# Kernel tuning notes

Hardware: AMD Instinct MI355X
Metric: run time of the kernel (lower is better)

## Reference

```python
import jax, jax.numpy as jnp
import numpy as np

B, IN, COND, H, LAT, E, GH = 8192, 256, 1024, 1024, 128, 6, 64
INP = LAT + COND      # decoder layer0 input size = 1152
INTER = LAT + H       # decoder layer1/2 input size = 1152


def setup_inputs() -> dict:
    key = jax.random.key(0)
    ks = jax.random.split(key, 30)
    n = lambda k, shape, s=0.02: jax.random.normal(k, shape, dtype=jnp.float32) * s
    return {
        'x': jax.random.normal(ks[0], (B, IN), dtype=jnp.float32),
        'y': jax.random.normal(ks[1], (B, COND), dtype=jnp.float32),
        'eps': jax.random.normal(ks[2], (B, LAT), dtype=jnp.float32),
        # encoder: layer k input = prev_dim + IN (x is re-concatenated each layer)
        'enc_w0': n(ks[3], (IN + COND + IN, H)), 'enc_b0': jnp.zeros((H,), jnp.float32),
        'enc_w1': n(ks[4], (H + IN, H)),         'enc_b1': jnp.zeros((H,), jnp.float32),
        'mu_w': n(ks[5], (H, LAT)),  'mu_b': jnp.zeros((LAT,), jnp.float32),
        'lv_w': n(ks[6], (H, LAT)),  'lv_b': jnp.zeros((LAT,), jnp.float32),
        # gating network (input = latent + cond)
        'g_w0': n(ks[7], (INP, GH)), 'g_b0': jnp.zeros((GH,), jnp.float32),
        'g_w1': n(ks[8], (GH, GH)),  'g_b1': jnp.zeros((GH,), jnp.float32),
        'g_w2': n(ks[9], (GH, E)),   'g_b2': jnp.zeros((E,), jnp.float32),
        # expert weights [E, in, out] and biases [E, out] (bias init 0.01 as in source)
        'exp_w0': n(ks[10], (E, INP, H)),   'exp_b0': jnp.full((E, H), 0.01, jnp.float32),
        'exp_w1': n(ks[11], (E, INTER, H)), 'exp_b1': jnp.full((E, H), 0.01, jnp.float32),
        'exp_w2': n(ks[12], (E, INTER, IN)), 'exp_b2': jnp.full((E, IN), 0.01, jnp.float32),
    }


def _forward(x, y, eps, enc_w0, enc_b0, enc_w1, enc_b1, mu_w, mu_b, lv_w, lv_b,
             g_w0, g_b0, g_w1, g_b1, g_w2, g_b2,
             exp_w0, exp_b0, exp_w1, exp_b1, exp_w2, exp_b2):
    elu = jax.nn.elu
    # --- Encoder ---
    h = jnp.concatenate([x, y], axis=1)
    h = elu(jnp.concatenate([h, x], axis=1) @ enc_w0 + enc_b0)
    h = elu(jnp.concatenate([h, x], axis=1) @ enc_w1 + enc_b1)
    mu = h @ mu_w + mu_b
    logvar = h @ lv_w + lv_b
    # --- Reparameterize (eps passed explicitly for determinism) ---
    z = mu + eps * jnp.exp(0.5 * logvar)
    # --- MixedDecoder ---
    g = jnp.concatenate([z, y], axis=1)
    g = elu(g @ g_w0 + g_b0)
    g = elu(g @ g_w1 + g_b1)
    coeff = jax.nn.softmax(g @ g_w2 + g_b2, axis=1)  # [B, E]
    layer_out = y
    for W, bb, act in ((exp_w0, exp_b0, True), (exp_w1, exp_b1, True), (exp_w2, exp_b2, False)):
        inp = jnp.concatenate([z, layer_out], axis=1)  # [B, I]
        # fused mixture-of-experts projection: avoids materializing per-sample [B,I,O] weight
        out = coeff @ bb + jnp.einsum('be,bi,eio->bo', coeff, inp, W)
        layer_out = elu(out) if act else out
    return layer_out, mu, logvar


def reference(x, y, eps, enc_w0, enc_b0, enc_w1, enc_b1, mu_w, mu_b, lv_w, lv_b,
              g_w0, g_b0, g_w1, g_b1, g_w2, g_b2,
              exp_w0, exp_b0, exp_w1, exp_b1, exp_w2, exp_b2):
    return _forward(x, y, eps, enc_w0, enc_b0, enc_w1, enc_b1, mu_w, mu_b, lv_w, lv_b,
                    g_w0, g_b0, g_w1, g_b1, g_w2, g_b2,
                    exp_w0, exp_b0, exp_w1, exp_b1, exp_w2, exp_b2)
```

## Files before the change

kernel.cpp:

```cpp
#include <hip/hip_runtime.h>
#include <hip/hip_bf16.h>
#include <cstddef>

using u16 = unsigned short;
using short8 = __attribute__((ext_vector_type(8))) short;
using f32x4 = __attribute__((ext_vector_type(4))) float;

constexpr int B_   = 8192;
constexpr int IN_  = 256;
constexpr int COND_= 1024;
constexpr int H_   = 1024;
constexpr int LAT_ = 128;
constexpr int NE_  = 6;
constexpr int GH_  = 64;
constexpr int INP_ = 1152;
constexpr int K0_  = 1536;
constexpr int K1_  = 1280;

constexpr int BK = 64;

typedef const __attribute__((address_space(1))) void gv_t;
typedef __attribute__((address_space(3))) void lv_t;
#define GLDS(g, l) __builtin_amdgcn_global_load_lds((gv_t*)(g), (lv_t*)(l), 16, 0, 0)

__device__ __forceinline__ u16 f2b(float f) {
  __hip_bfloat16 h = __float2bfloat16(f);
  return *reinterpret_cast<u16*>(&h);
}
__device__ __forceinline__ float elu1(float x) { return x > 0.f ? x : (__expf(x) - 1.f); }

__global__ void k_transpose(const float* __restrict__ in, u16* __restrict__ out,
                            int R, int C, long inStride, long outStride) {
  __shared__ float t[32][33];
  const float* ip = in + (long)blockIdx.z * inStride;
  u16* op = out + (long)blockIdx.z * outStride;
  int c0 = blockIdx.x * 32, r0 = blockIdx.y * 32;
  int tx = threadIdx.x, ty = threadIdx.y;
#pragma unroll
  for (int i = 0; i < 4; i++) {
    int r = r0 + ty + i * 8, c = c0 + tx;
    if (r < R && c < C) t[ty + i * 8][tx] = ip[(long)r * C + c];
  }
  __syncthreads();
#pragma unroll
  for (int i = 0; i < 4; i++) {
    int c = c0 + ty + i * 8, r = r0 + tx;
    if (r < R && c < C) op[(long)c * R + r] = f2b(t[tx][ty + i * 8]);
  }
}

__global__ __launch_bounds__(256) void k_pre(
    const float* __restrict__ enc_w0, const float* __restrict__ enc_w1,
    const float* __restrict__ mu_w, const float* __restrict__ lv_w,
    const float* __restrict__ g_w0, const float* __restrict__ exp_w0,
    const float* __restrict__ x, const float* __restrict__ y,
    u16* __restrict__ encw0T, u16* __restrict__ encw1T, u16* __restrict__ mulvT,
    u16* __restrict__ gw0T, u16* __restrict__ ew0T,
    u16* __restrict__ A0, u16* __restrict__ A1)
{
  __shared__ float t[32][33];
  const int b = blockIdx.x;
  const int tid = threadIdx.x;
  const int tx = tid & 31, ty = tid >> 5;

  auto tr = [&](const float* in, u16* out, int R, int C, int bx, int by) {
    int c0 = bx * 32, r0 = by * 32;
#pragma unroll
    for (int i = 0; i < 4; i++) {
      int r = r0 + ty + i * 8, c = c0 + tx;
      if (r < R && c < C) t[ty + i * 8][tx] = in[(long)r * C + c];
    }
    __syncthreads();
#pragma unroll
    for (int i = 0; i < 4; i++) {
      int c = c0 + ty + i * 8, r = r0 + tx;
      if (r < R && c < C) out[(long)c * R + r] = f2b(t[tx][ty + i * 8]);
    }
  };

  if (b < 1536)       { tr(enc_w0, encw0T, K0_, H_, b & 31, b >> 5); }
  else if (b < 2816)  { int l = b - 1536; tr(enc_w1, encw1T, K1_, H_, l & 31, l >> 5); }
  else if (b < 2944)  { int l = b - 2816; tr(mu_w, mulvT, H_, LAT_, l & 3, l >> 2); }
  else if (b < 3072)  { int l = b - 2944; tr(lv_w, mulvT + (size_t)LAT_ * H_, H_, LAT_, l & 3, l >> 2); }
  else if (b < 3144)  { int l = b - 3072; tr(g_w0, gw0T, INP_, GH_, l & 1, l >> 1); }
  else if (b < 10056) {
    int l = b - 3144, e = l / 1152, r2 = l % 1152;
    tr(exp_w0 + (long)e * INP_ * H_, ew0T + (long)e * INP_ * H_, INP_, H_, r2 & 31, r2 >> 5);
  } else {
    long idx = (long)(b - 10056) * 256 + tid;
    long n0 = (long)B_ * K0_;
    if (idx < n0) {
      int bb = (int)(idx / K0_), c = (int)(idx % K0_);
      float v;
      if (c < IN_)              v = x[(long)bb * IN_ + c];
      else if (c < IN_ + COND_) v = y[(long)bb * COND_ + (c - IN_)];
      else                      v = x[(long)bb * IN_ + (c - IN_ - COND_)];
      A0[idx] = f2b(v);
    } else {
      long j = idx - n0;
      if (j < (long)B_ * IN_) {
        int bb = (int)(j / IN_), c = (int)(j % IN_);
        A1[(long)bb * K1_ + H_ + c] = f2b(x[(long)bb * IN_ + c]);
      }
    }
  }
}

__global__ __launch_bounds__(256) void k_mid(
    const float* __restrict__ exp_w2, u16* __restrict__ ew2T,
    const float* __restrict__ mu, const float* __restrict__ lv,
    const float* __restrict__ eps, const float* __restrict__ y,
    u16* __restrict__ ZY, u16* __restrict__ D1, u16* __restrict__ D2)
{
  __shared__ float t[32][33];
  const int b = blockIdx.x;
  const int tid = threadIdx.x;
  if (b < 1728) {
    const int tx = tid & 31, ty = tid >> 5;
    int e = b / 288, r2 = b % 288;
    const float* in = exp_w2 + (long)e * INP_ * IN_;
    u16* out = ew2T + (long)e * INP_ * IN_;
    int c0 = (r2 & 7) * 32, r0 = (r2 >> 3) * 32;
#pragma unroll
    for (int i = 0; i < 4; i++) {
      int r = r0 + ty + i * 8, c = c0 + tx;
      if (r < INP_ && c < IN_) t[ty + i * 8][tx] = in[(long)r * IN_ + c];
    }
    __syncthreads();
#pragma unroll
    for (int i = 0; i < 4; i++) {
      int c = c0 + ty + i * 8, r = r0 + tx;
      if (r < INP_ && c < IN_) out[(long)c * INP_ + r] = f2b(t[tx][ty + i * 8]);
    }
  } else {
    long idx = (long)(b - 1728) * 256 + tid;
    if (idx >= (long)B_ * INP_) return;
    int bb = (int)(idx / INP_), c = (int)(idx % INP_);
    if (c < LAT_) {
      long o = (long)bb * LAT_ + c;
      float z = mu[o] + eps[o] * __expf(0.5f * lv[o]);
      u16 zb = f2b(z);
      ZY[idx] = zb; D1[idx] = zb; D2[idx] = zb;
    } else {
      ZY[idx] = f2b(y[(long)bb * COND_ + (c - LAT_)]);
    }
  }
}

__global__ __launch_bounds__(256) void k_gate(const float* __restrict__ G1,
    const float* __restrict__ w1, const float* __restrict__ b1,
    const float* __restrict__ w2, const float* __restrict__ b2,
    float* __restrict__ coeff) {
  __shared__ float W1[64][65];
  __shared__ float W2[64][8];
  __shared__ float B1[64], B2[8];
  int tid = threadIdx.x;
  for (int i = tid; i < 64 * 64; i += 256) W1[i >> 6][i & 63] = w1[i];
  for (int i = tid; i < 64 * 6; i += 256) W2[i / 6][i % 6] = w2[i];
  if (tid < 64) B1[tid] = b1[tid];
  if (tid < 8)  B2[tid] = (tid < 6) ? b2[tid] : 0.f;
  __syncthreads();
  int row = blockIdx.x * 256 + tid;
  const float* gr = G1 + (long)row * GH_;
  float g[64];
#pragma unroll
  for (int i = 0; i < 16; i++) {
    float4 v = *(const float4*)(gr + i * 4);
    g[i*4] = v.x; g[i*4+1] = v.y; g[i*4+2] = v.z; g[i*4+3] = v.w;
  }
  float lg[6];
#pragma unroll
  for (int e = 0; e < 6; e++) lg[e] = B2[e];
  for (int n = 0; n < 64; n++) {
    float s = B1[n];
#pragma unroll
    for (int k = 0; k < 64; k++) s += g[k] * W1[k][n];
    s = elu1(s);
#pragma unroll
    for (int e = 0; e < 6; e++) lg[e] += s * W2[n][e];
  }
  float m = lg[0];
#pragma unroll
  for (int e = 1; e < 6; e++) m = fmaxf(m, lg[e]);
  float p[6], sum = 0.f;
#pragma unroll
  for (int e = 0; e < 6; e++) { p[e] = __expf(lg[e] - m); sum += p[e]; }
  float inv = 1.f / sum;
#pragma unroll
  for (int e = 0; e < 6; e++) coeff[(long)row * 6 + e] = p[e] * inv;
}

template<int KSTEPS, int E, bool MOE>
__global__ __launch_bounds__(512, 2) void k_gemm8(
    const u16* __restrict__ A,
    const u16* __restrict__ WT,
    const float* __restrict__ bias,
    const float* __restrict__ coeff,
    int N,
    u16* __restrict__ outH, int ldo)
{
  constexpr int KK = KSTEPS * BK;
  constexpr int T = E * KSTEPS;
  __shared__ __align__(16) u16 As[3][256][BK];
  __shared__ __align__(16) u16 Bs[3][128][BK];
  __shared__ float Cf[MOE ? 256 : 1][8];

  const int tid = threadIdx.x;
  const int lane = tid & 63, w = tid >> 6;
  const int wr = w >> 1, wc = w & 1;
  const int lin = blockIdx.x + blockIdx.y * gridDim.x;
  const int rb  = (lin & 7) * 4 + ((lin >> 3) & 3);
  const int cp  = lin >> 5;
  const int brow = rb * 256, bcol = cp * 128;
  const int lr = lane & 15, hi = lane >> 4;
  const int lk = hi * 8;
  const int xsw = (lr & 7) << 3;

  if (MOE) {
    if (tid < 256) {
#pragma unroll
      for (int e2 = 0; e2 < 8; e2++)
        Cf[tid][e2] = (e2 < 6) ? coeff[(long)(brow + tid) * 6 + e2] : 0.f;
    }
    __syncthreads();
  }

  f32x4 acc[4][4];
#pragma unroll
  for (int m = 0; m < 4; m++)
#pragma unroll
    for (int n = 0; n < 4; n++)
#pragma unroll
      for (int r = 0; r < 4; r++) acc[m][n][r] = 0.f;
  f32x4 pacc[MOE ? 4 : 1][MOE ? 4 : 1];
  if constexpr (MOE) {
#pragma unroll
    for (int m = 0; m < 4; m++)
#pragma unroll
      for (int n = 0; n < 4; n++)
#pragma unroll
        for (int r = 0; r < 4; r++) pacc[m][n][r] = 0.f;
  }

  const int srow = w * 8 + (lane >> 3);
  const int sdst = (lane & 7) * 8;
  const int ssrc = ((lane & 7) ^ ((lane >> 3) & 7)) * 8;
  const u16* Asrc = A + (long)(brow + srow) * KK + ssrc;
  const u16* Bsrc = WT + (long)(bcol + srow) * KK + ssrc;

  auto STAGE_H = [&](int t2, int buf, int h) {
    const int e2 = (E == 1) ? 0 : (t2 / KSTEPS);
    int k2 = (E == 1) ? t2 : (t2 % KSTEPS);
    if (E > 1 && (e2 & 1)) k2 = KSTEPS - 1 - k2;
    const u16* ap = Asrc + (long)k2 * BK;
    const u16* bp = Bsrc + (long)e2 * ((long)N * KK) + (long)k2 * BK;
    GLDS(ap + (long)((h * 2 + 0) * 64) * KK, &As[buf][(h * 2 + 0) * 64 + srow][sdst]);
    GLDS(ap + (long)((h * 2 + 1) * 64) * KK, &As[buf][(h * 2 + 1) * 64 + srow][sdst]);
    GLDS(bp + (long)(h * 64) * KK,           &Bs[buf][h * 64 + srow][sdst]);
  };

  STAGE_H(0, 0, 0); STAGE_H(0, 0, 1);
  STAGE_H(1, 1, 0); STAGE_H(1, 1, 1);
  asm volatile("s_waitcnt vmcnt(6)" ::: "memory");
  asm volatile("s_barrier" ::: "memory");

  for (int t = 0; t < T; ++t) {
    const int cur = t % 3;
    const int nbuf = (t + 2) % 3;
    const bool do_stage = (t + 2 < T);

    {
      short8 af[4], bfr[4];
      const int cc = lk ^ xsw;
#pragma unroll
      for (int m = 0; m < 4; m++)
        af[m] = *(const short8*)&As[cur][wr * 64 + m * 16 + lr][cc];
#pragma unroll
      for (int n = 0; n < 4; n++)
        bfr[n] = *(const short8*)&Bs[cur][wc * 64 + n * 16 + lr][cc];
      if (do_stage) STAGE_H(t + 2, nbuf, 0);
      asm volatile("s_barrier" ::: "memory");
      __builtin_amdgcn_s_setprio(1);
#pragma unroll
      for (int m = 0; m < 4; m++)
#pragma unroll
        for (int n = 0; n < 4; n++) {
          if constexpr (MOE)
            pacc[m][n] = __builtin_amdgcn_mfma_f32_16x16x32_bf16(af[m], bfr[n], pacc[m][n], 0, 0, 0);
          else
            acc[m][n] = __builtin_amdgcn_mfma_f32_16x16x32_bf16(af[m], bfr[n], acc[m][n], 0, 0, 0);
        }
      __builtin_amdgcn_s_setprio(0);
      asm volatile("s_barrier" ::: "memory");
    }

    {
      short8 af[4], bfr[4];
      const int cc = (32 + lk) ^ xsw;
#pragma unroll
      for (int m = 0; m < 4; m++)
        af[m] = *(const short8*)&As[cur][wr * 64 + m * 16 + lr][cc];
#pragma unroll
      for (int n = 0; n < 4; n++)
        bfr[n] = *(const short8*)&Bs[cur][wc * 64 + n * 16 + lr][cc];
      if (do_stage) STAGE_H(t + 2, nbuf, 1);
      asm volatile("s_barrier" ::: "memory");
      __builtin_amdgcn_s_setprio(1);
#pragma unroll
      for (int m = 0; m < 4; m++)
#pragma unroll
        for (int n = 0; n < 4; n++) {
          if constexpr (MOE)
            pacc[m][n] = __builtin_amdgcn_mfma_f32_16x16x32_bf16(af[m], bfr[n], pacc[m][n], 0, 0, 0);
          else
            acc[m][n] = __builtin_amdgcn_mfma_f32_16x16x32_bf16(af[m], bfr[n], acc[m][n], 0, 0, 0);
        }
      __builtin_amdgcn_s_setprio(0);
      if (t + 1 < T) {
        if (do_stage) asm volatile("s_waitcnt vmcnt(6)" ::: "memory");
        else          asm volatile("s_waitcnt vmcnt(0)" ::: "memory");
      }
      asm volatile("s_barrier" ::: "memory");
    }

    if constexpr (MOE) {
      if ((t + 1) % KSTEPS == 0) {
        const int e = t / KSTEPS;
#pragma unroll
        for (int m = 0; m < 4; m++)
#pragma unroll
          for (int r = 0; r < 4; r++) {
            float c = Cf[wr * 64 + m * 16 + hi * 4 + r][e];
#pragma unroll
            for (int n = 0; n < 4; n++) acc[m][n][r] += c * pacc[m][n][r];
          }
        if (t + 1 < T) {
#pragma unroll
          for (int m = 0; m < 4; m++)
#pragma unroll
            for (int n = 0; n < 4; n++)
#pragma unroll
              for (int r = 0; r < 4; r++) pacc[m][n][r] = 0.f;
        }
      }
    }
  }

#pragma unroll
  for (int m = 0; m < 4; m++)
#pragma unroll
    for (int n = 0; n < 4; n++) {
      const int col = bcol + wc * 64 + n * 16 + lr;
#pragma unroll
      for (int r = 0; r < 4; r++) {
        const int rowl = wr * 64 + m * 16 + hi * 4 + r;
        const long row = brow + rowl;
        float v = acc[m][n][r];
        if constexpr (MOE) {
          float bv = 0.f;
#pragma unroll
          for (int e = 0; e < 6; e++) bv += Cf[rowl][e] * bias[(long)e * N + col];
          v += bv;
        } else {
          v += bias[col];
        }
        v = elu1(v);
        outH[row * (long)ldo + col] = f2b(v);
      }
    }
}

template<int KSTEPS, int E, bool MOE>
__global__ __launch_bounds__(256, 2) void k_m2(
    const u16* __restrict__ A,
    const u16* __restrict__ WT,
    const float* __restrict__ bias, const float* __restrict__ bias2,
    const float* __restrict__ coeff,
    int N,
    u16* __restrict__ outH, float* __restrict__ outF, float* __restrict__ outF2,
    int ldo, int splitcol, int act)
{
  constexpr int KK = KSTEPS * BK;
  constexpr int T = E * KSTEPS;
  __shared__ __align__(16) u16 As[3][64][BK];
  __shared__ __align__(16) u16 Bs[3][128][BK];
  __shared__ float Cf[MOE ? 64 : 1][8];

  const int tid = threadIdx.x;
  const int lane = tid & 63, w = tid >> 6;
  const int wr = w >> 1, wc = w & 1;
  const int brow = blockIdx.x * 64, bcol = blockIdx.y * 128;
  const int lr = lane & 15, hi = lane >> 4;
  const int lk = hi * 8;
  const int xsw = (lr & 7) << 3;

  if (MOE) {
    if (tid < 64) {
#pragma unroll
      for (int e2 = 0; e2 < 8; e2++)
        Cf[tid][e2] = (e2 < 6) ? coeff[(long)(brow + tid) * 6 + e2] : 0.f;
    }
    __syncthreads();
  }

  f32x4 acc[2][4];
#pragma unroll
  for (int m = 0; m < 2; m++)
#pragma unroll
    for (int n = 0; n < 4; n++)
#pragma unroll
      for (int r = 0; r < 4; r++) acc[m][n][r] = 0.f;
  f32x4 pacc[MOE ? 2 : 1][MOE ? 4 : 1];
  if constexpr (MOE) {
#pragma unroll
    for (int m = 0; m < 2; m++)
#pragma unroll
      for (int n = 0; n < 4; n++)
#pragma unroll
        for (int r = 0; r < 4; r++) pacc[m][n][r] = 0.f;
  }

  const int srow = w * 8 + (lane >> 3);
  const int sdst = (lane & 7) * 8;
  const int ssrc = ((lane & 7) ^ ((lane >> 3) & 7)) * 8;
  const u16* Asrc = A + (long)(brow + srow) * KK + ssrc;
  const u16* Bsrc = WT + (long)(bcol + srow) * KK + ssrc;

  auto STAGE_H = [&](int t2, int buf, int h) {
    const int e2 = (E == 1) ? 0 : (t2 / KSTEPS);
    int k2 = (E == 1) ? t2 : (t2 % KSTEPS);
    if (E > 1 && (e2 & 1)) k2 = KSTEPS - 1 - k2;
    const u16* ap = Asrc + (long)k2 * BK;
    const u16* bp = Bsrc + (long)e2 * ((long)N * KK) + (long)k2 * BK;
    GLDS(ap + (long)(h * 32) * KK,            &As[buf][h * 32 + srow][sdst]);
    GLDS(bp + (long)(h * 64) * KK,            &Bs[buf][h * 64 + srow][sdst]);
    GLDS(bp + (long)(h * 64 + 32) * KK,       &Bs[buf][h * 64 + 32 + srow][sdst]);
  };

  STAGE_H(0, 0, 0); STAGE_H(0, 0, 1);
  STAGE_H(1, 1, 0); STAGE_H(1, 1, 1);
  asm volatile("s_waitcnt vmcnt(6)" ::: "memory");
  asm volatile("s_barrier" ::: "memory");

  for (int t = 0; t < T; ++t) {
    const int cur = t % 3;
    const int nbuf = (t + 2) % 3;
    const bool do_stage = (t + 2 < T);

    {
      short8 af[2], bfr[4];
      const int cc = lk ^ xsw;
#pragma unroll
      for (int m = 0; m < 2; m++)
        af[m] = *(const short8*)&As[cur][wr * 32 + m * 16 + lr][cc];
#pragma unroll
      for (int n = 0; n < 4; n++)
        bfr[n] = *(const short8*)&Bs[cur][wc * 64 + n * 16 + lr][cc];
      if (do_stage) STAGE_H(t + 2, nbuf, 0);
      asm volatile("s_barrier" ::: "memory");
      __builtin_amdgcn_s_setprio(1);
#pragma unroll
      for (int m = 0; m < 2; m++)
#pragma unroll
        for (int n = 0; n < 4; n++) {
          if constexpr (MOE)
            pacc[m][n] = __builtin_amdgcn_mfma_f32_16x16x32_bf16(af[m], bfr[n], pacc[m][n], 0, 0, 0);
          else
            acc[m][n] = __builtin_amdgcn_mfma_f32_16x16x32_bf16(af[m], bfr[n], acc[m][n], 0, 0, 0);
        }
      __builtin_amdgcn_s_setprio(0);
      asm volatile("s_barrier" ::: "memory");
    }

    {
      short8 af[2], bfr[4];
      const int cc = (32 + lk) ^ xsw;
#pragma unroll
      for (int m = 0; m < 2; m++)
        af[m] = *(const short8*)&As[cur][wr * 32 + m * 16 + lr][cc];
#pragma unroll
      for (int n = 0; n < 4; n++)
        bfr[n] = *(const short8*)&Bs[cur][wc * 64 + n * 16 + lr][cc];
      if (do_stage) STAGE_H(t + 2, nbuf, 1);
      asm volatile("s_barrier" ::: "memory");
      __builtin_amdgcn_s_setprio(1);
#pragma unroll
      for (int m = 0; m < 2; m++)
#pragma unroll
        for (int n = 0; n < 4; n++) {
          if constexpr (MOE)
            pacc[m][n] = __builtin_amdgcn_mfma_f32_16x16x32_bf16(af[m], bfr[n], pacc[m][n], 0, 0, 0);
          else
            acc[m][n] = __builtin_amdgcn_mfma_f32_16x16x32_bf16(af[m], bfr[n], acc[m][n], 0, 0, 0);
        }
      __builtin_amdgcn_s_setprio(0);
      if (t + 1 < T) {
        if (do_stage) asm volatile("s_waitcnt vmcnt(6)" ::: "memory");
        else          asm volatile("s_waitcnt vmcnt(0)" ::: "memory");
      }
      asm volatile("s_barrier" ::: "memory");
    }

    if constexpr (MOE) {
      if ((t + 1) % KSTEPS == 0) {
        const int e = t / KSTEPS;
#pragma unroll
        for (int m = 0; m < 2; m++)
#pragma unroll
          for (int r = 0; r < 4; r++) {
            float c = Cf[wr * 32 + m * 16 + hi * 4 + r][e];
#pragma unroll
            for (int n = 0; n < 4; n++) acc[m][n][r] += c * pacc[m][n][r];
          }
        if (t + 1 < T) {
#pragma unroll
          for (int m = 0; m < 2; m++)
#pragma unroll
            for (int n = 0; n < 4; n++)
#pragma unroll
              for (int r = 0; r < 4; r++) pacc[m][n][r] = 0.f;
        }
      }
    }
  }

#pragma unroll
  for (int m = 0; m < 2; m++)
#pragma unroll
    for (int n = 0; n < 4; n++) {
      const int col = bcol + wc * 64 + n * 16 + lr;
      if (col >= N) continue;
#pragma unroll
      for (int r = 0; r < 4; r++) {
        const int rowl = wr * 32 + m * 16 + hi * 4 + r;
        const long row = brow + rowl;
        float v = acc[m][n][r];
        if constexpr (MOE) {
          float bv = 0.f;
#pragma unroll
          for (int e = 0; e < 6; e++) bv += Cf[rowl][e] * bias[(long)e * N + col];
          v += bv;
        } else {
          v += (col < splitcol) ? bias[col] : bias2[col - splitcol];
        }
        if (act) v = elu1(v);
        if (outH) outH[row * (long)ldo + col] = f2b(v);
        else if (col < splitcol) outF[row * (long)ldo + col] = v;
        else outF2[row * (long)ldo + (col - splitcol)] = v;
      }
    }
}

extern "C" void kernel_launch(void* const* d_in, const int* in_sizes, int n_in,
                              void* d_out, int out_size, void* d_ws, size_t ws_size,
                              hipStream_t stream) {
  (void)in_sizes; (void)out_size;
  if (n_in < 23) return;
  const float* x      = (const float*)d_in[0];
  const float* y      = (const float*)d_in[1];
  const float* eps    = (const float*)d_in[2];
  const float* enc_w0 = (const float*)d_in[3];
  const float* enc_b0 = (const float*)d_in[4];
  const float* enc_w1 = (const float*)d_in[5];
  const float* enc_b1 = (const float*)d_in[6];
  const float* mu_w   = (const float*)d_in[7];
  const float* mu_b   = (const float*)d_in[8];
  const float* lv_w   = (const float*)d_in[9];
  const float* lv_b   = (const float*)d_in[10];
  const float* g_w0   = (const float*)d_in[11];
  const float* g_b0   = (const float*)d_in[12];
  const float* g_w1   = (const float*)d_in[13];
  const float* g_b1   = (const float*)d_in[14];
  const float* g_w2   = (const float*)d_in[15];
  const float* g_b2   = (const float*)d_in[16];
  const float* exp_w0 = (const float*)d_in[17];
  const float* exp_b0 = (const float*)d_in[18];
  const float* exp_w1 = (const float*)d_in[19];
  const float* exp_b1 = (const float*)d_in[20];
  const float* exp_w2 = (const float*)d_in[21];
  const float* exp_b2 = (const float*)d_in[22];

  char* ws = (char*)d_ws;
  size_t off = 0;
  auto alloc = [&](size_t bytes) -> void* {
    void* p = ws + off; off += (bytes + 255) & ~(size_t)255; return p;
  };
  u16* A0     = (u16*)alloc((size_t)B_ * K0_ * 2);
  u16* A1     = (u16*)alloc((size_t)B_ * K1_ * 2);
  u16* H2     = (u16*)alloc((size_t)B_ * H_ * 2);
  u16* ZY     = (u16*)alloc((size_t)B_ * INP_ * 2);
  u16* encw0T = (u16*)alloc((size_t)K0_ * H_ * 2);
  u16* encw1T = (u16*)alloc((size_t)K1_ * H_ * 2);
  u16* mulvT  = (u16*)alloc((size_t)256 * H_ * 2);
  u16* gw0T   = (u16*)alloc((size_t)GH_ * INP_ * 2);
  u16* ew0T   = (u16*)alloc((size_t)NE_ * H_ * INP_ * 2);
  if (ws_size < off) return;

  u16* D1 = A0;
  u16* D2 = A1;
  float* G1    = (float*)H2;
  float* COEFF = (float*)((char*)H2 + (size_t)B_ * GH_ * 4);
  u16* ew2T = (u16*)((char*)H2 + (size_t)4 * 1024 * 1024);
  u16* ew1T = ZY;

  float* outO = (float*)d_out;
  float* muO  = outO + (size_t)B_ * IN_;
  float* lvO  = muO + (size_t)B_ * LAT_;

  k_pre<<<67400, 256, 0, stream>>>(enc_w0, enc_w1, mu_w, lv_w, g_w0, exp_w0,
      x, y, encw0T, encw1T, mulvT, gw0T, ew0T, A0, A1);

  k_gemm8<K0_ / BK, 1, false><<<dim3(32, 8), 512, 0, stream>>>(A0, encw0T, enc_b0,
      nullptr, H_, A1, K1_);
  k_gemm8<K1_ / BK, 1, false><<<dim3(32, 8), 512, 0, stream>>>(A1, encw1T, enc_b1,
      nullptr, H_, H2, H_);

  k_m2<H_ / BK, 1, false><<<dim3(B_ / 64, 2), 256, 0, stream>>>(H2, mulvT,
      mu_b, lv_b, nullptr, 256, nullptr, muO, lvO, LAT_, LAT_, 0);

  k_mid<<<38592, 256, 0, stream>>>(exp_w2, ew2T, muO, lvO, eps, y, ZY, D1, D2);

  k_m2<INP_ / BK, 1, false><<<dim3(B_ / 64, 1), 256, 0, stream>>>(ZY, gw0T,
      g_b0, g_b0, nullptr, GH_, nullptr, G1, nullptr, GH_, GH_, 1);
  k_gate<<<B_ / 256, 256, 0, stream>>>(G1, g_w1, g_b1, g_w2, g_b2, COEFF);

  k_gemm8<INP_ / BK, NE_, true><<<dim3(32, 8), 512, 0, stream>>>(ZY, ew0T, exp_b0,
      COEFF, H_, D1 + LAT_, INP_);
  k_transpose<<<dim3(32, 36, NE_), dim3(32, 8), 0, stream>>>(exp_w1, ew1T, INP_, H_,
                                                    (long)INP_ * H_, (long)INP_ * H_);
  k_gemm8<INP_ / BK, NE_, true><<<dim3(32, 8), 512, 0, stream>>>(D1, ew1T, exp_b1,
      COEFF, H_, D2 + LAT_, INP_);
  k_m2<INP_ / BK, NE_, true><<<dim3(B_ / 64, 2), 256, 0, stream>>>(D2, ew2T,
      exp_b2, nullptr, COEFF, IN_, nullptr, outO, nullptr, IN_, IN_, 0);
}
```

Before: 533.5 us.

## Reorder MoE GEMM loop to share A tile across experts per k-step

The mixture-of-experts GEMM moves the expert loop inside the k loop. Each A tile is loaded into LDS once and reused by all six experts, instead of being reloaded once per expert. The per-expert partial product is scaled by the gating coefficient and added to the accumulator after every k-step, which adds VALU FMAs and a coefficient LDS read per step. A is now double-buffered and B triple-buffered, which changes the LDS footprint and the vmcnt waits.

```diff
diff --git a/kernel.cpp b/kernel.cpp
--- a/kernel.cpp
+++ b/kernel.cpp
@@ -190,8 +190,8 @@
   for (int e = 0; e < 6; e++) coeff[(long)row * 6 + e] = p[e] * inv;
 }
 
-template<int KSTEPS, int E, bool MOE>
-__global__ __launch_bounds__(512, 2) void k_gemm8(
+template<int KSTEPS>
+__global__ __launch_bounds__(512, 2) void k_moe8(
     const u16* __restrict__ A,
     const u16* __restrict__ WT,
     const float* __restrict__ bias,
@@ -200,10 +200,9 @@
     u16* __restrict__ outH, int ldo)
 {
   constexpr int KK = KSTEPS * BK;
-  constexpr int T = E * KSTEPS;
-  __shared__ __align__(16) u16 As[3][256][BK];
+  __shared__ __align__(16) u16 As[2][256][BK];
   __shared__ __align__(16) u16 Bs[3][128][BK];
-  __shared__ float Cf[MOE ? 256 : 1][8];
+  __shared__ float CfT[6][256];
 
   const int tid = threadIdx.x;
   const int lane = tid & 63, w = tid >> 6;
@@ -216,14 +215,11 @@
   const int lk = hi * 8;
   const int xsw = (lr & 7) << 3;
 
-  if (MOE) {
-    if (tid < 256) {
-#pragma unroll
-      for (int e2 = 0; e2 < 8; e2++)
-        Cf[tid][e2] = (e2 < 6) ? coeff[(long)(brow + tid) * 6 + e2] : 0.f;
-    }
-    __syncthreads();
-  }
+  if (tid < 256) {
+#pragma unroll
+    for (int e = 0; e < 6; e++) CfT[e][tid] = coeff[(long)(brow + tid) * 6 + e];
+  }
+  __syncthreads();
 
   f32x4 acc[4][4];
 #pragma unroll
@@ -232,15 +228,8 @@
     for (int n = 0; n < 4; n++)
 #pragma unroll
       for (int r = 0; r < 4; r++) acc[m][n][r] = 0.f;
-  f32x4 pacc[MOE ? 4 : 1][MOE ? 4 : 1];
-  if constexpr (MOE) {
-#pragma unroll
-    for (int m = 0; m < 4; m++)
-#pragma unroll
-      for (int n = 0; n < 4; n++)
-#pragma unroll
-        for (int r = 0; r < 4; r++) pacc[m][n][r] = 0.f;
-  }
+  const f32x4 zf = {0.f, 0.f, 0.f, 0.f};
+  f32x4 pacc[4][4];
 
   const int srow = w * 8 + (lane >> 3);
   const int sdst = (lane & 7) * 8;
@@ -248,12 +237,162 @@
   const u16* Asrc = A + (long)(brow + srow) * KK + ssrc;
   const u16* Bsrc = WT + (long)(bcol + srow) * KK + ssrc;
 
+  auto STAGE_A = [&](int kt2, int abuf2) {
+    const u16* ap = Asrc + (long)kt2 * BK;
+#pragma unroll
+    for (int i = 0; i < 4; i++)
+      GLDS(ap + (long)(i * 64) * KK, &As[abuf2][i * 64 + srow][sdst]);
+  };
+  auto STAGE_B = [&](int e2, int k2, int buf) {
+    const u16* bp = Bsrc + (long)e2 * ((long)N * KK) + (long)k2 * BK;
+    GLDS(bp,                 &Bs[buf][srow][sdst]);
+    GLDS(bp + (long)64 * KK, &Bs[buf][64 + srow][sdst]);
+  };
+
+  STAGE_A(0, 0);
+  STAGE_B(0, 0, 0);
+  STAGE_B(1, 0, 1);
+  asm volatile("s_waitcnt vmcnt(2)" ::: "memory");
+  asm volatile("s_barrier" ::: "memory");
+
+  short8 af[2][4];
+
+  for (int kt = 0; kt < KSTEPS; ++kt) {
+    const int abuf = kt & 1;
+    const bool haveA = (kt + 1 < KSTEPS);
+#pragma unroll
+    for (int g = 0; g < 6; ++g) {
+      const int cur = g % 3;
+      const int nbuf = (g + 2) % 3;
+      const int e2 = (g + 2) % 6;
+      const int k2 = kt + (g >= 4 ? 1 : 0);
+      const bool stageB = (k2 < KSTEPS);
+
+      float4 cg[4];
+      {
+        if (g == 0) {
+#pragma unroll
+          for (int p = 0; p < 2; p++)
+#pragma unroll
+            for (int m = 0; m < 4; m++)
+              af[p][m] = *(const short8*)&As[abuf][wr * 64 + m * 16 + lr][(p * 32 + lk) ^ xsw];
+        }
+#pragma unroll
+        for (int m = 0; m < 4; m++)
+          cg[m] = *(const float4*)&CfT[g][wr * 64 + m * 16 + hi * 4];
+        short8 bfr[4];
+        const int cc0 = lk ^ xsw;
+#pragma unroll
+        for (int n = 0; n < 4; n++)
+          bfr[n] = *(const short8*)&Bs[cur][wc * 64 + n * 16 + lr][cc0];
+        if (stageB) STAGE_B(e2, k2, nbuf);
+        if (g == 2 && haveA) STAGE_A(kt + 1, abuf ^ 1);
+        asm volatile("s_barrier" ::: "memory");
+        __builtin_amdgcn_s_setprio(1);
+#pragma unroll
+        for (int m = 0; m < 4; m++)
+#pragma unroll
+          for (int n = 0; n < 4; n++)
+            pacc[m][n] = __builtin_amdgcn_mfma_f32_16x16x32_bf16(af[0][m], bfr[n], zf, 0, 0, 0);
+        __builtin_amdgcn_s_setprio(0);
+        asm volatile("s_barrier" ::: "memory");
+      }
+      {
+        short8 bfr[4];
+        const int cc1 = (32 + lk) ^ xsw;
+#pragma unroll
+        for (int n = 0; n < 4; n++)
+          bfr[n] = *(const short8*)&Bs[cur][wc * 64 + n * 16 + lr][cc1];
+        asm volatile("s_barrier" ::: "memory");
+        __builtin_amdgcn_s_setprio(1);
+#pragma unroll
+        for (int m = 0; m < 4; m++)
+#pragma unroll
+          for (int n = 0; n < 4; n++)
+            pacc[m][n] = __builtin_amdgcn_mfma_f32_16x16x32_bf16(af[1][m], bfr[n], pacc[m][n], 0, 0, 0);
+        __builtin_amdgcn_s_setprio(0);
+        if (stageB) {
+          if ((g == 2 || g == 3) && haveA)
+            asm volatile("s_waitcnt vmcnt(6)" ::: "memory");
+          else
+            asm volatile("s_waitcnt vmcnt(2)" ::: "memory");
+        } else if (g == 4) {
+          asm volatile("s_waitcnt vmcnt(0)" ::: "memory");
+        }
+        asm volatile("s_barrier" ::: "memory");
+      }
+#pragma unroll
+      for (int m = 0; m < 4; m++)
+#pragma unroll
+        for (int r = 0; r < 4; r++) {
+          const float c = cg[m][r];
+#pragma unroll
+          for (int n = 0; n < 4; n++) acc[m][n][r] += c * pacc[m][n][r];
+        }
+    }
+  }
+
+#pragma unroll
+  for (int m = 0; m < 4; m++)
+#pragma unroll
+    for (int n = 0; n < 4; n++) {
+      const int col = bcol + wc * 64 + n * 16 + lr;
+#pragma unroll
+      for (int r = 0; r < 4; r++) {
+        const int rowl = wr * 64 + m * 16 + hi * 4 + r;
+        const long row = brow + rowl;
+        float v = acc[m][n][r];
+        float bv = 0.f;
+#pragma unroll
+        for (int e = 0; e < 6; e++) bv += CfT[e][rowl] * bias[(long)e * N + col];
+        v += bv;
+        v = elu1(v);
+        outH[row * (long)ldo + col] = f2b(v);
+      }
+    }
+}
+
+template<int KSTEPS>
+__global__ __launch_bounds__(512, 2) void k_gemm8(
+    const u16* __restrict__ A,
+    const u16* __restrict__ WT,
+    const float* __restrict__ bias,
+    int N,
+    u16* __restrict__ outH, int ldo)
+{
+  constexpr int KK = KSTEPS * BK;
+  constexpr int T = KSTEPS;
+  __shared__ __align__(16) u16 As[3][256][BK];
+  __shared__ __align__(16) u16 Bs[3][128][BK];
+
+  const int tid = threadIdx.x;
+  const int lane = tid & 63, w = tid >> 6;
+  const int wr = w >> 1, wc = w & 1;
+  const int lin = blockIdx.x + blockIdx.y * gridDim.x;
+  const int rb  = (lin & 7) * 4 + ((lin >> 3) & 3);
+  const int cp  = lin >> 5;
+  const int brow = rb * 256, bcol = cp * 128;
+  const int lr = lane & 15, hi = lane >> 4;
+  const int lk = hi * 8;
+  const int xsw = (lr & 7) << 3;
+
+  f32x4 acc[4][4];
+#pragma unroll
+  for (int m = 0; m < 4; m++)
+#pragma unroll
+    for (int n = 0; n < 4; n++)
+#pragma unroll
+      for (int r = 0; r < 4; r++) acc[m][n][r] = 0.f;
+
+  const int srow = w * 8 + (lane >> 3);
+  const int sdst = (lane & 7) * 8;
+  const int ssrc = ((lane & 7) ^ ((lane >> 3) & 7)) * 8;
+  const u16* Asrc = A + (long)(brow + srow) * KK + ssrc;
+  const u16* Bsrc = WT + (long)(bcol + srow) * KK + ssrc;
+
   auto STAGE_H = [&](int t2, int buf, int h) {
-    const int e2 = (E == 1) ? 0 : (t2 / KSTEPS);
-    int k2 = (E == 1) ? t2 : (t2 % KSTEPS);
-    if (E > 1 && (e2 & 1)) k2 = KSTEPS - 1 - k2;
-    const u16* ap = Asrc + (long)k2 * BK;
-    const u16* bp = Bsrc + (long)e2 * ((long)N * KK) + (long)k2 * BK;
+    const u16* ap = Asrc + (long)t2 * BK;
+    const u16* bp = Bsrc + (long)t2 * BK;
     GLDS(ap + (long)((h * 2 + 0) * 64) * KK, &As[buf][(h * 2 + 0) * 64 + srow][sdst]);
     GLDS(ap + (long)((h * 2 + 1) * 64) * KK, &As[buf][(h * 2 + 1) * 64 + srow][sdst]);
     GLDS(bp + (long)(h * 64) * KK,           &Bs[buf][h * 64 + srow][sdst]);
@@ -284,16 +423,11 @@
 #pragma unroll
       for (int m = 0; m < 4; m++)
 #pragma unroll
-        for (int n = 0; n < 4; n++) {
-          if constexpr (MOE)
-            pacc[m][n] = __builtin_amdgcn_mfma_f32_16x16x32_bf16(af[m], bfr[n], pacc[m][n], 0, 0, 0);
-          else
-            acc[m][n] = __builtin_amdgcn_mfma_f32_16x16x32_bf16(af[m], bfr[n], acc[m][n], 0, 0, 0);
-        }
+        for (int n = 0; n < 4; n++)
+          acc[m][n] = __builtin_amdgcn_mfma_f32_16x16x32_bf16(af[m], bfr[n], acc[m][n], 0, 0, 0);
       __builtin_amdgcn_s_setprio(0);
       asm volatile("s_barrier" ::: "memory");
     }
-
     {
       short8 af[4], bfr[4];
       const int cc = (32 + lk) ^ xsw;
@@ -309,12 +443,8 @@
 #pragma unroll
       for (int m = 0; m < 4; m++)
 #pragma unroll
-        for (int n = 0; n < 4; n++) {
-          if constexpr (MOE)
-            pacc[m][n] = __builtin_amdgcn_mfma_f32_16x16x32_bf16(af[m], bfr[n], pacc[m][n], 0, 0, 0);
-          else
-            acc[m][n] = __builtin_amdgcn_mfma_f32_16x16x32_bf16(af[m], bfr[n], acc[m][n], 0, 0, 0);
-        }
+        for (int n = 0; n < 4; n++)
+          acc[m][n] = __builtin_amdgcn_mfma_f32_16x16x32_bf16(af[m], bfr[n], acc[m][n], 0, 0, 0);
       __builtin_amdgcn_s_setprio(0);
       if (t + 1 < T) {
         if (do_stage) asm volatile("s_waitcnt vmcnt(6)" ::: "memory");
@@ -322,28 +452,6 @@
       }
       asm volatile("s_barrier" ::: "memory");
     }
-
-    if constexpr (MOE) {
-      if ((t + 1) % KSTEPS == 0) {
-        const int e = t / KSTEPS;
-#pragma unroll
-        for (int m = 0; m < 4; m++)
-#pragma unroll
-          for (int r = 0; r < 4; r++) {
-            float c = Cf[wr * 64 + m * 16 + hi * 4 + r][e];
-#pragma unroll
-            for (int n = 0; n < 4; n++) acc[m][n][r] += c * pacc[m][n][r];
-          }
-        if (t + 1 < T) {
-#pragma unroll
-          for (int m = 0; m < 4; m++)
-#pragma unroll
-            for (int n = 0; n < 4; n++)
-#pragma unroll
-              for (int r = 0; r < 4; r++) pacc[m][n][r] = 0.f;
-        }
-      }
-    }
   }
 
 #pragma unroll
@@ -355,15 +463,7 @@
       for (int r = 0; r < 4; r++) {
         const int rowl = wr * 64 + m * 16 + hi * 4 + r;
         const long row = brow + rowl;
-        float v = acc[m][n][r];
-        if constexpr (MOE) {
-          float bv = 0.f;
-#pragma unroll
-          for (int e = 0; e < 6; e++) bv += Cf[rowl][e] * bias[(long)e * N + col];
-          v += bv;
-        } else {
-          v += bias[col];
-        }
+        float v = acc[m][n][r] + bias[col];
         v = elu1(v);
         outH[row * (long)ldo + col] = f2b(v);
       }
@@ -471,7 +571,6 @@
       __builtin_amdgcn_s_setprio(0);
       asm volatile("s_barrier" ::: "memory");
     }
-
     {
       short8 af[2], bfr[4];
       const int cc = (32 + lk) ^ xsw;
@@ -610,10 +709,8 @@
   k_pre<<<67400, 256, 0, stream>>>(enc_w0, enc_w1, mu_w, lv_w, g_w0, exp_w0,
       x, y, encw0T, encw1T, mulvT, gw0T, ew0T, A0, A1);
 
-  k_gemm8<K0_ / BK, 1, false><<<dim3(32, 8), 512, 0, stream>>>(A0, encw0T, enc_b0,
-      nullptr, H_, A1, K1_);
-  k_gemm8<K1_ / BK, 1, false><<<dim3(32, 8), 512, 0, stream>>>(A1, encw1T, enc_b1,
-      nullptr, H_, H2, H_);
+  k_gemm8<K0_ / BK><<<dim3(32, 8), 512, 0, stream>>>(A0, encw0T, enc_b0, H_, A1, K1_);
+  k_gemm8<K1_ / BK><<<dim3(32, 8), 512, 0, stream>>>(A1, encw1T, enc_b1, H_, H2, H_);
 
   k_m2<H_ / BK, 1, false><<<dim3(B_ / 64, 2), 256, 0, stream>>>(H2, mulvT,
       mu_b, lv_b, nullptr, 256, nullptr, muO, lvO, LAT_, LAT_, 0);
@@ -624,11 +721,11 @@
       g_b0, g_b0, nullptr, GH_, nullptr, G1, nullptr, GH_, GH_, 1);
   k_gate<<<B_ / 256, 256, 0, stream>>>(G1, g_w1, g_b1, g_w2, g_b2, COEFF);
 
-  k_gemm8<INP_ / BK, NE_, true><<<dim3(32, 8), 512, 0, stream>>>(ZY, ew0T, exp_b0,
+  k_moe8<INP_ / BK><<<dim3(32, 8), 512, 0, stream>>>(ZY, ew0T, exp_b0,
       COEFF, H_, D1 + LAT_, INP_);
   k_transpose<<<dim3(32, 36, NE_), dim3(32, 8), 0, stream>>>(exp_w1, ew1T, INP_, H_,
                                                     (long)INP_ * H_, (long)INP_ * H_);
-  k_gemm8<INP_ / BK, NE_, true><<<dim3(32, 8), 512, 0, stream>>>(D1, ew1T, exp_b1,
+  k_moe8<INP_ / BK><<<dim3(32, 8), 512, 0, stream>>>(D1, ew1T, exp_b1,
       COEFF, H_, D2 + LAT_, INP_);
   k_m2<INP_ / BK, NE_, true><<<dim3(B_ / 64, 2), 256, 0, stream>>>(D2, ew2T,
       exp_b2, nullptr, COEFF, IN_, nullptr, outO, nullptr, IN_, IN_, 0);
```

Result: slower. 784.7 us (+47.1%).
